# Performance work log

Measured on AMD Instinct MI355X. Metric: run time of the kernel, lower is better.

## Reference

```python
import jax, jax.numpy as jnp
import numpy as np

FP8_MAX = 448.0   # torch.finfo(float8_e4m3fn).max
BLK = 128         # block_size = [128, 128] for weights; [1, 128] for activations
E, H, I, T, TOPK = 8, 2048, 1408, 512, 2
FP8 = jnp.float8_e4m3fn


def fp8_round(x):
    """Round-trip through float8_e4m3fn (simulates .to(float8_e4m3fn))."""
    return jnp.clip(x, -FP8_MAX, FP8_MAX).astype(FP8).astype(jnp.float32)


def setup_inputs() -> dict:
    key = jax.random.key(0)
    ks = jax.random.split(key, 7)
    hidden_states = jax.random.normal(ks[0], (T, H), jnp.float32)
    top_k_index = jax.random.randint(ks[1], (T, TOPK), 0, E)
    top_k_weights = jax.random.uniform(ks[2], (T, TOPK), jnp.float32)
    # FP8 weight codes (stored as fp32 values exactly representable in e4m3fn)
    gate_up_proj = fp8_round(jax.random.normal(ks[3], (E, 2 * I, H), jnp.float32))
    gate_up_proj_scale_inv = jax.random.uniform(ks[4], (E, (2 * I) // BLK, H // BLK), jnp.float32, 1e-4, 1e-2)
    down_proj = fp8_round(jax.random.normal(ks[5], (E, H, I), jnp.float32))
    down_proj_scale_inv = jax.random.uniform(ks[6], (E, H // BLK, I // BLK), jnp.float32, 1e-4, 1e-2)
    return {
        "hidden_states": hidden_states,
        "top_k_index": top_k_index,
        "top_k_weights": top_k_weights,
        "gate_up_proj": gate_up_proj,
        "gate_up_proj_scale_inv": gate_up_proj_scale_inv,
        "down_proj": down_proj,
        "down_proj_scale_inv": down_proj_scale_inv,
    }


def dequant_weight(wq, s):
    # wq: [E, N, K] fp8 codes; s: [E, N//BLK, K//BLK] per-128x128-block scale_inv
    e, n, k = wq.shape
    wb = wq.reshape(e, n // BLK, BLK, k // BLK, BLK)
    return (wb * s[:, :, None, :, None]).reshape(e, n, k)


def quant_dequant_act(x):
    # dynamic per-(row, 128-block) fp8 activation quantization, then dequant
    shp = x.shape
    xb = x.reshape(shp[:-1] + (shp[-1] // BLK, BLK))
    amax = jnp.max(jnp.abs(xb), axis=-1, keepdims=True)
    scale = jnp.maximum(amax, 1e-12) / FP8_MAX
    q = fp8_round(xb / scale)
    return (q * scale).reshape(shp)


def reference(hidden_states, top_k_index, top_k_weights, gate_up_proj,
              gate_up_proj_scale_inv, down_proj, down_proj_scale_inv):
    w_gu = dequant_weight(gate_up_proj, gate_up_proj_scale_inv)  # [E, 2I, H]
    w_d = dequant_weight(down_proj, down_proj_scale_inv)         # [E, H, I]
    # activation quantization is per-token-block, so unrouted tokens are
    # unaffected; dense per-expert compute + combine-weight mask equals the
    # original gather/scatter loop exactly (unrouted contributions weight 0).
    x = quant_dequant_act(hidden_states)                         # [T, H]
    gate_up = jnp.einsum('th,enh->etn', x, w_gu)                 # [E, T, 2I]
    gate, up = jnp.split(gate_up, 2, axis=-1)
    h = jax.nn.silu(gate) * up                                   # [E, T, I]
    h = quant_dequant_act(h)
    down = jnp.einsum('eti,ehi->eth', h, w_d)                    # [E, T, H]
    # combine[t, e] = sum over top-k slots routing token t to expert e
    combine = jnp.sum(jax.nn.one_hot(top_k_index, E, dtype=top_k_weights.dtype)
                      * top_k_weights[..., None], axis=1)        # [T, E]
    out = jnp.einsum('eth,te->th', down, combine)
    return out.astype(hidden_states.dtype)
```

## Files before the change

### kernel.cpp

```cpp
#include <hip/hip_runtime.h>
#include <math.h>

#define NE 8
#define HD 2048
#define ID 1408
#define NT 512
#define FP8MAX 448.0f

typedef __attribute__((ext_vector_type(4))) float floatx4;

__device__ __forceinline__ floatx4 fzero4() {
    floatx4 z; z.x = 0.f; z.y = 0.f; z.z = 0.f; z.w = 0.f; return z;
}

#define OFF_OFFS  0
#define OFF_TOK   1024
#define OFF_WGT   8192
#define OFF_ENT   16384
#define OFF_XSG   32768
#define OFF_XG    131072
#define OFF_HS    (3*1024*1024)
#define OFF_HQ    (3*1024*1024 + 65536)
#define OFF_GU0   (5*1024*1024)
#define OFF_GU1   (17*1024*1024)

#define LDA 136

__global__ void route_kernel(const int* __restrict__ tki,
                             const float* __restrict__ tkw,
                             int* __restrict__ offs,
                             int* __restrict__ tok,
                             float* __restrict__ wgt,
                             int* __restrict__ ent) {
    __shared__ int cnt[NE];
    __shared__ int cur[NE];
    __shared__ int base[NE + 1];
    int tid = threadIdx.x;
    if (tid < NE) { cnt[tid] = 0; cur[tid] = 0; }
    __syncthreads();
    int e = tki[tid];
    atomicAdd(&cnt[e], 1);
    __syncthreads();
    if (tid == 0) {
        int s = 0;
        for (int i = 0; i < NE; i++) { base[i] = s; s += cnt[i]; }
        base[NE] = s;
    }
    __syncthreads();
    int pos = atomicAdd(&cur[e], 1);
    int j = base[e] + pos;
    tok[j] = tid >> 1;
    wgt[j] = tkw[tid];
    ent[tid] = j;
    if (tid <= NE) offs[tid] = base[tid];
}

__global__ void quant_x_kernel(const float* __restrict__ x,
                               const int* __restrict__ ent,
                               unsigned char* __restrict__ xg,
                               float* __restrict__ xsg) {
    int wid = (blockIdx.x * 256 + threadIdx.x) >> 6;
    int lane = threadIdx.x & 63;
    int t = wid >> 4;
    int b = wid & 15;
    const float2 v = *(const float2*)(x + (long)t * HD + b * 128 + lane * 2);
    float am = fmaxf(fabsf(v.x), fabsf(v.y));
    #pragma unroll
    for (int m = 32; m; m >>= 1) am = fmaxf(am, __shfl_xor(am, m));
    float scale = fmaxf(am, 1e-12f) / FP8MAX;
    int p = __builtin_amdgcn_cvt_pk_fp8_f32(v.x / scale, v.y / scale, 0, false);
    unsigned short pk = (unsigned short)(p & 0xffff);
    int e0 = ent[2 * t], e1 = ent[2 * t + 1];
    *(unsigned short*)(xg + (long)e0 * HD + b * 128 + lane * 2) = pk;
    *(unsigned short*)(xg + (long)e1 * HD + b * 128 + lane * 2) = pk;
    if (lane == 0) { xsg[e0 * 16 + b] = scale; xsg[e1 * 16 + b] = scale; }
}

__global__ void quant_h_kernel(const float* __restrict__ gu0,
                               const float* __restrict__ gu1,
                               unsigned char* __restrict__ hq,
                               float* __restrict__ hs) {
    int wid = (blockIdx.x * 256 + threadIdx.x) >> 6;
    int lane = threadIdx.x & 63;
    int j = wid / 11;
    int b = wid - j * 11;
    long base = (long)j * 2816 + b * 128 + lane * 2;
    float2 ga = *(const float2*)(gu0 + base);
    float2 gb = *(const float2*)(gu1 + base);
    float2 ua = *(const float2*)(gu0 + base + 1408);
    float2 ub = *(const float2*)(gu1 + base + 1408);
    float gx = ga.x + gb.x, gy = ga.y + gb.y;
    float ux = ua.x + ub.x, uy = ua.y + ub.y;
    float hx = (gx / (1.0f + expf(-gx))) * ux;
    float hy = (gy / (1.0f + expf(-gy))) * uy;
    float am = fmaxf(fabsf(hx), fabsf(hy));
    #pragma unroll
    for (int m = 32; m; m >>= 1) am = fmaxf(am, __shfl_xor(am, m));
    float scale = fmaxf(am, 1e-12f) / FP8MAX;
    int p = __builtin_amdgcn_cvt_pk_fp8_f32(hx / scale, hy / scale, 0, false);
    *(unsigned short*)(hq + (long)j * ID + b * 128 + lane * 2) =
        (unsigned short)(p & 0xffff);
    if (lane == 0) hs[j * 11 + b] = scale;
}

__global__ __launch_bounds__(256, 4) void gemm1_kernel(
    const unsigned char* __restrict__ xg,
    const float* __restrict__ xsg,
    const float* __restrict__ wgu,
    const float* __restrict__ sgu,
    const int* __restrict__ offs,
    float* __restrict__ gu0,
    float* __restrict__ gu1) {
    int e = blockIdx.z;
    int jb = blockIdx.x >> 1;
    int kh = blockIdx.x & 1;
    int o0 = offs[e], o1 = offs[e + 1];
    int ne = o1 - o0;
    if (ne <= 0) return;

    __shared__ __align__(16) unsigned char Asm[128 * LDA];
    __shared__ __align__(16) unsigned char Bsm[64 * LDA];
    __shared__ __align__(16) float sxa[128 * 20];

    int tid = threadIdx.x;
    int wave = tid >> 6;
    int lane = tid & 63;
    int lr = lane & 15;
    int lq = lane >> 4;

    int bcol = tid & 31;
    int brow0 = tid >> 5;
    const float* bG = wgu + ((long)e * 2816 + jb * 32 + brow0) * HD + bcol * 4;
    const float* bU = wgu + ((long)e * 2816 + 1408 + jb * 32 + brow0) * HD + bcol * 4;
    const float* sgp = sgu + (e * 22 + (jb >> 2)) * 16;
    const float* sup = sgu + (e * 22 + 11 + (jb >> 2)) * 16;

    int aseg = tid & 7;
    int arow0 = tid >> 3;
    int kbS = kh * 8, kbE = kbS + 8;

    for (int m0 = 0; m0 < ne; m0 += 128) {
        int rem = ne - m0;
        int j0 = o0 + m0;

        {
            int r = tid >> 1, q = tid & 1;
            int j = j0 + r; if (j >= o1) j = o0;
            float4 s0 = *(const float4*)(xsg + j * 16 + q * 8);
            float4 s1 = *(const float4*)(xsg + j * 16 + q * 8 + 4);
            *(float4*)&sxa[r * 20 + q * 8] = s0;
            *(float4*)&sxa[r * 20 + q * 8 + 4] = s1;
        }

        const unsigned char* aBase0;
        const unsigned char* aBase1;
        const unsigned char* aBase2;
        const unsigned char* aBase3;
        {
            int j;
            j = j0 + arow0;       if (j >= o1) j = o0; aBase0 = xg + (long)j * HD + aseg * 16;
            j = j0 + 32 + arow0;  if (j >= o1) j = o0; aBase1 = xg + (long)j * HD + aseg * 16;
            j = j0 + 64 + arow0;  if (j >= o1) j = o0; aBase2 = xg + (long)j * HD + aseg * 16;
            j = j0 + 96 + arow0;  if (j >= o1) j = o0; aBase3 = xg + (long)j * HD + aseg * 16;
        }

        floatx4 facc[8];
        #pragma unroll
        for (int i = 0; i < 8; i++) facc[i] = fzero4();

        for (int kb = kbS; kb < kbE; kb++) {
            {
                uint4 a0 = *(const uint4*)(aBase0 + kb * 128);
                uint4 a1 = *(const uint4*)(aBase1 + kb * 128);
                uint4 a2 = *(const uint4*)(aBase2 + kb * 128);
                uint4 a3 = *(const uint4*)(aBase3 + kb * 128);
                float4 f0 = *(const float4*)(bG + kb * 128);
                float4 f1 = *(const float4*)(bG + kb * 128 + 8 * HD);
                float4 f2 = *(const float4*)(bG + kb * 128 + 16 * HD);
                float4 f3 = *(const float4*)(bG + kb * 128 + 24 * HD);
                float4 f4 = *(const float4*)(bU + kb * 128);
                float4 f5 = *(const float4*)(bU + kb * 128 + 8 * HD);
                float4 f6 = *(const float4*)(bU + kb * 128 + 16 * HD);
                float4 f7 = *(const float4*)(bU + kb * 128 + 24 * HD);
                *(uint4*)(&Asm[(arow0)      * LDA + aseg * 16]) = a0;
                *(uint4*)(&Asm[(arow0 + 32) * LDA + aseg * 16]) = a1;
                *(uint4*)(&Asm[(arow0 + 64) * LDA + aseg * 16]) = a2;
                *(uint4*)(&Asm[(arow0 + 96) * LDA + aseg * 16]) = a3;
                int p0 = __builtin_amdgcn_cvt_pk_fp8_f32(f0.x, f0.y, 0, false);
                p0 = __builtin_amdgcn_cvt_pk_fp8_f32(f0.z, f0.w, p0, true);
                int p1 = __builtin_amdgcn_cvt_pk_fp8_f32(f1.x, f1.y, 0, false);
                p1 = __builtin_amdgcn_cvt_pk_fp8_f32(f1.z, f1.w, p1, true);
                int p2 = __builtin_amdgcn_cvt_pk_fp8_f32(f2.x, f2.y, 0, false);
                p2 = __builtin_amdgcn_cvt_pk_fp8_f32(f2.z, f2.w, p2, true);
                int p3 = __builtin_amdgcn_cvt_pk_fp8_f32(f3.x, f3.y, 0, false);
                p3 = __builtin_amdgcn_cvt_pk_fp8_f32(f3.z, f3.w, p3, true);
                int p4 = __builtin_amdgcn_cvt_pk_fp8_f32(f4.x, f4.y, 0, false);
                p4 = __builtin_amdgcn_cvt_pk_fp8_f32(f4.z, f4.w, p4, true);
                int p5 = __builtin_amdgcn_cvt_pk_fp8_f32(f5.x, f5.y, 0, false);
                p5 = __builtin_amdgcn_cvt_pk_fp8_f32(f5.z, f5.w, p5, true);
                int p6 = __builtin_amdgcn_cvt_pk_fp8_f32(f6.x, f6.y, 0, false);
                p6 = __builtin_amdgcn_cvt_pk_fp8_f32(f6.z, f6.w, p6, true);
                int p7 = __builtin_amdgcn_cvt_pk_fp8_f32(f7.x, f7.y, 0, false);
                p7 = __builtin_amdgcn_cvt_pk_fp8_f32(f7.z, f7.w, p7, true);
                *(unsigned int*)(&Bsm[(brow0)      * LDA + bcol * 4]) = (unsigned int)p0;
                *(unsigned int*)(&Bsm[(brow0 + 8)  * LDA + bcol * 4]) = (unsigned int)p1;
                *(unsigned int*)(&Bsm[(brow0 + 16) * LDA + bcol * 4]) = (unsigned int)p2;
                *(unsigned int*)(&Bsm[(brow0 + 24) * LDA + bcol * 4]) = (unsigned int)p3;
                *(unsigned int*)(&Bsm[(brow0 + 32) * LDA + bcol * 4]) = (unsigned int)p4;
                *(unsigned int*)(&Bsm[(brow0 + 40) * LDA + bcol * 4]) = (unsigned int)p5;
                *(unsigned int*)(&Bsm[(brow0 + 48) * LDA + bcol * 4]) = (unsigned int)p6;
                *(unsigned int*)(&Bsm[(brow0 + 56) * LDA + bcol * 4]) = (unsigned int)p7;
            }
            __syncthreads();
            floatx4 cacc[8];
            #pragma unroll
            for (int i = 0; i < 8; i++) cacc[i] = fzero4();
            #pragma unroll
            for (int ks = 0; ks < 4; ks++) {
                long a[2], b[4];
                #pragma unroll
                for (int mi = 0; mi < 2; mi++)
                    a[mi] = *(const long*)(&Asm[(wave * 32 + mi * 16 + lr) * LDA + ks * 32 + lq * 8]);
                #pragma unroll
                for (int ni = 0; ni < 4; ni++)
                    b[ni] = *(const long*)(&Bsm[(ni * 16 + lr) * LDA + ks * 32 + lq * 8]);
                #pragma unroll
                for (int mi = 0; mi < 2; mi++)
                    #pragma unroll
                    for (int ni = 0; ni < 4; ni++)
                        cacc[mi * 4 + ni] = __builtin_amdgcn_mfma_f32_16x16x32_fp8_fp8(
                            a[mi], b[ni], cacc[mi * 4 + ni], 0, 0, 0);
            }
            float sg = sgp[kb];
            float su = sup[kb];
            #pragma unroll
            for (int mi = 0; mi < 2; mi++) {
                #pragma unroll
                for (int reg = 0; reg < 4; reg++) {
                    float sx = sxa[(wave * 32 + mi * 16 + lq * 4 + reg) * 20 + kb];
                    #pragma unroll
                    for (int ni = 0; ni < 4; ni++) {
                        float sw = (ni < 2) ? sg : su;
                        facc[mi * 4 + ni][reg] += cacc[mi * 4 + ni][reg] * (sw * sx);
                    }
                }
            }
            __syncthreads();
        }

        float* gu = kh ? gu1 : gu0;
        #pragma unroll
        for (int mi = 0; mi < 2; mi++) {
            #pragma unroll
            for (int ni = 0; ni < 4; ni++) {
                #pragma unroll
                for (int reg = 0; reg < 4; reg++) {
                    int r = wave * 32 + mi * 16 + lq * 4 + reg;
                    if (r < rem) {
                        long base = (long)(j0 + r) * 2816;
                        long col = (ni < 2) ? (jb * 32 + ni * 16 + lr)
                                            : (1408 + jb * 32 + (ni - 2) * 16 + lr);
                        gu[base + col] = facc[mi * 4 + ni][reg];
                    }
                }
            }
        }
    }
}

__global__ __launch_bounds__(256, 4) void gemm2_kernel(
    const unsigned char* __restrict__ hq,
    const float* __restrict__ hs,
    const float* __restrict__ wd,
    const float* __restrict__ sd,
    const int* __restrict__ offs,
    float* __restrict__ d0,
    float* __restrict__ d1) {
    int e = blockIdx.z;
    int jb = blockIdx.x >> 1;
    int kh = blockIdx.x & 1;
    int o0 = offs[e], o1 = offs[e + 1];
    int ne = o1 - o0;
    if (ne <= 0) return;

    __shared__ __align__(16) unsigned char Asm[128 * LDA];
    __shared__ __align__(16) unsigned char Bsm[32 * LDA];
    __shared__ __align__(16) float sha[128 * 12];

    int tid = threadIdx.x;
    int wave = tid >> 6;
    int lane = tid & 63;
    int lr = lane & 15;
    int lq = lane >> 4;

    int aseg = tid & 7;
    int arow0 = tid >> 3;

    int bcol = tid & 31;
    int brow0 = tid >> 5;
    const float* bB = wd + ((long)e * HD + jb * 32 + brow0) * ID + bcol * 4;
    const float* sdp = sd + (e * 16 + (jb >> 2)) * 11;

    int kb0 = kh ? 6 : 0, kb1 = kh ? 11 : 6;
    float* dp = kh ? d1 : d0;

    for (int m0 = 0; m0 < ne; m0 += 128) {
        int rem = ne - m0;
        int j0 = o0 + m0;

        if (tid < 128) {
            int j = j0 + tid;
            if (j >= o1) j = o0;
            const float* s = hs + j * 11;
            #pragma unroll
            for (int k = 0; k < 11; k++) sha[tid * 12 + k] = s[k];
        }

        const unsigned char* aBase0;
        const unsigned char* aBase1;
        const unsigned char* aBase2;
        const unsigned char* aBase3;
        {
            int j;
            j = j0 + arow0;       if (j >= o1) j = o0; aBase0 = hq + (long)j * ID + aseg * 16;
            j = j0 + 32 + arow0;  if (j >= o1) j = o0; aBase1 = hq + (long)j * ID + aseg * 16;
            j = j0 + 64 + arow0;  if (j >= o1) j = o0; aBase2 = hq + (long)j * ID + aseg * 16;
            j = j0 + 96 + arow0;  if (j >= o1) j = o0; aBase3 = hq + (long)j * ID + aseg * 16;
        }

        floatx4 facc[4];
        #pragma unroll
        for (int i = 0; i < 4; i++) facc[i] = fzero4();

        for (int kb = kb0; kb < kb1; kb++) {
            {
                uint4 a0 = *(const uint4*)(aBase0 + kb * 128);
                uint4 a1 = *(const uint4*)(aBase1 + kb * 128);
                uint4 a2 = *(const uint4*)(aBase2 + kb * 128);
                uint4 a3 = *(const uint4*)(aBase3 + kb * 128);
                float4 f0 = *(const float4*)(bB + kb * 128);
                float4 f1 = *(const float4*)(bB + kb * 128 + 8 * ID);
                float4 f2 = *(const float4*)(bB + kb * 128 + 16 * ID);
                float4 f3 = *(const float4*)(bB + kb * 128 + 24 * ID);
                *(uint4*)(&Asm[(arow0)      * LDA + aseg * 16]) = a0;
                *(uint4*)(&Asm[(arow0 + 32) * LDA + aseg * 16]) = a1;
                *(uint4*)(&Asm[(arow0 + 64) * LDA + aseg * 16]) = a2;
                *(uint4*)(&Asm[(arow0 + 96) * LDA + aseg * 16]) = a3;
                int p0 = __builtin_amdgcn_cvt_pk_fp8_f32(f0.x, f0.y, 0, false);
                p0 = __builtin_amdgcn_cvt_pk_fp8_f32(f0.z, f0.w, p0, true);
                int p1 = __builtin_amdgcn_cvt_pk_fp8_f32(f1.x, f1.y, 0, false);
                p1 = __builtin_amdgcn_cvt_pk_fp8_f32(f1.z, f1.w, p1, true);
                int p2 = __builtin_amdgcn_cvt_pk_fp8_f32(f2.x, f2.y, 0, false);
                p2 = __builtin_amdgcn_cvt_pk_fp8_f32(f2.z, f2.w, p2, true);
                int p3 = __builtin_amdgcn_cvt_pk_fp8_f32(f3.x, f3.y, 0, false);
                p3 = __builtin_amdgcn_cvt_pk_fp8_f32(f3.z, f3.w, p3, true);
                *(unsigned int*)(&Bsm[(brow0)      * LDA + bcol * 4]) = (unsigned int)p0;
                *(unsigned int*)(&Bsm[(brow0 + 8)  * LDA + bcol * 4]) = (unsigned int)p1;
                *(unsigned int*)(&Bsm[(brow0 + 16) * LDA + bcol * 4]) = (unsigned int)p2;
                *(unsigned int*)(&Bsm[(brow0 + 24) * LDA + bcol * 4]) = (unsigned int)p3;
            }
            __syncthreads();
            floatx4 cacc[4];
            #pragma unroll
            for (int i = 0; i < 4; i++) cacc[i] = fzero4();
            #pragma unroll
            for (int ks = 0; ks < 4; ks++) {
                long a[2], b[2];
                #pragma unroll
                for (int mi = 0; mi < 2; mi++)
                    a[mi] = *(const long*)(&Asm[(wave * 32 + mi * 16 + lr) * LDA + ks * 32 + lq * 8]);
                #pragma unroll
                for (int ni = 0; ni < 2; ni++)
                    b[ni] = *(const long*)(&Bsm[(ni * 16 + lr) * LDA + ks * 32 + lq * 8]);
                #pragma unroll
                for (int mi = 0; mi < 2; mi++)
                    #pragma unroll
                    for (int ni = 0; ni < 2; ni++)
                        cacc[mi * 2 + ni] = __builtin_amdgcn_mfma_f32_16x16x32_fp8_fp8(
                            a[mi], b[ni], cacc[mi * 2 + ni], 0, 0, 0);
            }
            float sw = sdp[kb];
            #pragma unroll
            for (int mi = 0; mi < 2; mi++) {
                #pragma unroll
                for (int reg = 0; reg < 4; reg++) {
                    float sh = sha[(wave * 32 + mi * 16 + lq * 4 + reg) * 12 + kb];
                    #pragma unroll
                    for (int ni = 0; ni < 2; ni++)
                        facc[mi * 2 + ni][reg] += cacc[mi * 2 + ni][reg] * (sw * sh);
                }
            }
            __syncthreads();
        }

        #pragma unroll
        for (int mi = 0; mi < 2; mi++) {
            #pragma unroll
            for (int ni = 0; ni < 2; ni++) {
                #pragma unroll
                for (int reg = 0; reg < 4; reg++) {
                    int r = wave * 32 + mi * 16 + lq * 4 + reg;
                    if (r < rem) {
                        dp[(long)(j0 + r) * HD + jb * 32 + ni * 16 + lr] =
                            facc[mi * 2 + ni][reg];
                    }
                }
            }
        }
    }
}

__global__ void combine_kernel(const float* __restrict__ d0,
                               const float* __restrict__ d1,
                               const int* __restrict__ ent,
                               const float* __restrict__ tkw,
                               float* __restrict__ out) {
    int gid = blockIdx.x * 256 + threadIdx.x;
    int t = gid >> 9;
    int c4 = gid & 511;
    int j0 = ent[2 * t], j1 = ent[2 * t + 1];
    float w0 = tkw[2 * t], w1 = tkw[2 * t + 1];
    long b0 = (long)j0 * HD + c4 * 4;
    long b1 = (long)j1 * HD + c4 * 4;
    float4 a0 = *(const float4*)(d0 + b0);
    float4 a1 = *(const float4*)(d1 + b0);
    float4 a2 = *(const float4*)(d0 + b1);
    float4 a3 = *(const float4*)(d1 + b1);
    float4 r;
    r.x = w0 * (a0.x + a1.x) + w1 * (a2.x + a3.x);
    r.y = w0 * (a0.y + a1.y) + w1 * (a2.y + a3.y);
    r.z = w0 * (a0.z + a1.z) + w1 * (a2.z + a3.z);
    r.w = w0 * (a0.w + a1.w) + w1 * (a2.w + a3.w);
    *(float4*)(out + (long)t * HD + c4 * 4) = r;
}

extern "C" void kernel_launch(void* const* d_in, const int* in_sizes, int n_in,
                              void* d_out, int out_size, void* d_ws, size_t ws_size,
                              hipStream_t stream) {
    (void)in_sizes; (void)n_in; (void)out_size; (void)ws_size;
    const float* x   = (const float*)d_in[0];
    const int*   tki = (const int*)d_in[1];
    const float* tkw = (const float*)d_in[2];
    const float* wgu = (const float*)d_in[3];
    const float* sgu = (const float*)d_in[4];
    const float* wd  = (const float*)d_in[5];
    const float* sd  = (const float*)d_in[6];
    float* out = (float*)d_out;
    char* ws = (char*)d_ws;

    int*   offs = (int*)(ws + OFF_OFFS);
    int*   tok  = (int*)(ws + OFF_TOK);
    float* wgt  = (float*)(ws + OFF_WGT);
    int*   ent  = (int*)(ws + OFF_ENT);
    float* xsg  = (float*)(ws + OFF_XSG);
    unsigned char* xg = (unsigned char*)(ws + OFF_XG);
    float* hs   = (float*)(ws + OFF_HS);
    unsigned char* hq = (unsigned char*)(ws + OFF_HQ);
    float* gu0  = (float*)(ws + OFF_GU0);
    float* gu1  = (float*)(ws + OFF_GU1);
    float* dp0  = (float*)(ws + OFF_GU0);
    float* dp1  = (float*)(ws + OFF_GU1);

    route_kernel<<<1, 1024, 0, stream>>>(tki, tkw, offs, tok, wgt, ent);
    quant_x_kernel<<<2048, 256, 0, stream>>>(x, ent, xg, xsg);
    gemm1_kernel<<<dim3(88, 1, NE), 256, 0, stream>>>(xg, xsg, wgu, sgu, offs, gu0, gu1);
    quant_h_kernel<<<2816, 256, 0, stream>>>(gu0, gu1, hq, hs);
    gemm2_kernel<<<dim3(128, 1, NE), 256, 0, stream>>>(hq, hs, wd, sd, offs, dp0, dp1);
    combine_kernel<<<1024, 256, 0, stream>>>(dp0, dp1, ent, tkw, out);
}
```

Before: 381.3 us.

## Pre-convert weights to fp8 in a separate pass and split M tiles across the grid

Adds a grid-stride kernel that converts both fp32 weight tensors to packed fp8 in workspace on every call. Both GEMMs then load 16-byte fp8 rows directly instead of fp32 loads plus in-loop conversion. The serial per-expert M-tile loop is replaced by a grid y dimension of 8 tiles, which adds more blocks for parallelism. The trade-off is one extra full pass over the weights, reading about 276 MB of fp32 and writing fp8, plus extra workspace.

```diff
diff --git a/kernel.cpp b/kernel.cpp
--- a/kernel.cpp
+++ b/kernel.cpp
@@ -23,6 +23,8 @@
 #define OFF_HQ    (3*1024*1024 + 65536)
 #define OFF_GU0   (5*1024*1024)
 #define OFF_GU1   (17*1024*1024)
+#define OFF_WGU8  (29L*1024*1024)
+#define OFF_WD8   (76L*1024*1024)
 
 #define LDA 136
 
@@ -55,6 +57,29 @@
     if (tid <= NE) offs[tid] = base[tid];
 }
 
+__global__ void quant_w_kernel(const float* __restrict__ wgu,
+                               const float* __restrict__ wd,
+                               unsigned int* __restrict__ wgu8,
+                               unsigned int* __restrict__ wd8) {
+    const long NGU4 = (long)NE * 2816 * 2048 / 4;
+    const long ND4  = (long)NE * HD * ID / 4;
+    long stride = (long)gridDim.x * 256;
+    for (long i = (long)blockIdx.x * 256 + threadIdx.x; i < NGU4 + ND4; i += stride) {
+        if (i < NGU4) {
+            float4 v = ((const float4*)wgu)[i];
+            int p = __builtin_amdgcn_cvt_pk_fp8_f32(v.x, v.y, 0, false);
+            p = __builtin_amdgcn_cvt_pk_fp8_f32(v.z, v.w, p, true);
+            wgu8[i] = (unsigned int)p;
+        } else {
+            long k = i - NGU4;
+            float4 v = ((const float4*)wd)[k];
+            int p = __builtin_amdgcn_cvt_pk_fp8_f32(v.x, v.y, 0, false);
+            p = __builtin_amdgcn_cvt_pk_fp8_f32(v.z, v.w, p, true);
+            wd8[k] = (unsigned int)p;
+        }
+    }
+}
+
 __global__ void quant_x_kernel(const float* __restrict__ x,
                                const int* __restrict__ ent,
                                unsigned char* __restrict__ xg,
@@ -106,162 +131,131 @@
 __global__ __launch_bounds__(256, 4) void gemm1_kernel(
     const unsigned char* __restrict__ xg,
     const float* __restrict__ xsg,
-    const float* __restrict__ wgu,
+    const unsigned char* __restrict__ wgu8,
     const float* __restrict__ sgu,
     const int* __restrict__ offs,
     float* __restrict__ gu0,
     float* __restrict__ gu1) {
     int e = blockIdx.z;
+    int mt = blockIdx.y;
     int jb = blockIdx.x >> 1;
     int kh = blockIdx.x & 1;
     int o0 = offs[e], o1 = offs[e + 1];
     int ne = o1 - o0;
-    if (ne <= 0) return;
+    int m0 = mt * 128;
+    if (m0 >= ne) return;
+    int rem = ne - m0;
+    int j0 = o0 + m0;
 
     __shared__ __align__(16) unsigned char Asm[128 * LDA];
     __shared__ __align__(16) unsigned char Bsm[64 * LDA];
     __shared__ __align__(16) float sxa[128 * 20];
 
     int tid = threadIdx.x;
+    {
+        int r = tid >> 1, q = tid & 1;
+        int j = j0 + r; if (j >= o1) j = o0;
+        float4 s0 = *(const float4*)(xsg + j * 16 + q * 8);
+        float4 s1 = *(const float4*)(xsg + j * 16 + q * 8 + 4);
+        *(float4*)&sxa[r * 20 + q * 8] = s0;
+        *(float4*)&sxa[r * 20 + q * 8 + 4] = s1;
+    }
+
     int wave = tid >> 6;
     int lane = tid & 63;
     int lr = lane & 15;
     int lq = lane >> 4;
 
-    int bcol = tid & 31;
-    int brow0 = tid >> 5;
-    const float* bG = wgu + ((long)e * 2816 + jb * 32 + brow0) * HD + bcol * 4;
-    const float* bU = wgu + ((long)e * 2816 + 1408 + jb * 32 + brow0) * HD + bcol * 4;
+    int aseg = tid & 7;
+    int arow0 = tid >> 3;
+    const unsigned char* aBase0;
+    const unsigned char* aBase1;
+    const unsigned char* aBase2;
+    const unsigned char* aBase3;
+    {
+        int j;
+        j = j0 + arow0;       if (j >= o1) j = o0; aBase0 = xg + (long)j * HD + aseg * 16;
+        j = j0 + 32 + arow0;  if (j >= o1) j = o0; aBase1 = xg + (long)j * HD + aseg * 16;
+        j = j0 + 64 + arow0;  if (j >= o1) j = o0; aBase2 = xg + (long)j * HD + aseg * 16;
+        j = j0 + 96 + arow0;  if (j >= o1) j = o0; aBase3 = xg + (long)j * HD + aseg * 16;
+    }
+
+    const unsigned char* bG8 = wgu8 + ((long)e * 2816 + jb * 32 + arow0) * HD + aseg * 16;
+    const unsigned char* bU8 = wgu8 + ((long)e * 2816 + 1408 + jb * 32 + arow0) * HD + aseg * 16;
     const float* sgp = sgu + (e * 22 + (jb >> 2)) * 16;
     const float* sup = sgu + (e * 22 + 11 + (jb >> 2)) * 16;
 
-    int aseg = tid & 7;
-    int arow0 = tid >> 3;
+    floatx4 facc[8];
+    #pragma unroll
+    for (int i = 0; i < 8; i++) facc[i] = fzero4();
+
     int kbS = kh * 8, kbE = kbS + 8;
 
-    for (int m0 = 0; m0 < ne; m0 += 128) {
-        int rem = ne - m0;
-        int j0 = o0 + m0;
-
+    for (int kb = kbS; kb < kbE; kb++) {
         {
-            int r = tid >> 1, q = tid & 1;
-            int j = j0 + r; if (j >= o1) j = o0;
-            float4 s0 = *(const float4*)(xsg + j * 16 + q * 8);
-            float4 s1 = *(const float4*)(xsg + j * 16 + q * 8 + 4);
-            *(float4*)&sxa[r * 20 + q * 8] = s0;
-            *(float4*)&sxa[r * 20 + q * 8 + 4] = s1;
-        }
-
-        const unsigned char* aBase0;
-        const unsigned char* aBase1;
-        const unsigned char* aBase2;
-        const unsigned char* aBase3;
-        {
-            int j;
-            j = j0 + arow0;       if (j >= o1) j = o0; aBase0 = xg + (long)j * HD + aseg * 16;
-            j = j0 + 32 + arow0;  if (j >= o1) j = o0; aBase1 = xg + (long)j * HD + aseg * 16;
-            j = j0 + 64 + arow0;  if (j >= o1) j = o0; aBase2 = xg + (long)j * HD + aseg * 16;
-            j = j0 + 96 + arow0;  if (j >= o1) j = o0; aBase3 = xg + (long)j * HD + aseg * 16;
-        }
-
-        floatx4 facc[8];
-        #pragma unroll
-        for (int i = 0; i < 8; i++) facc[i] = fzero4();
-
-        for (int kb = kbS; kb < kbE; kb++) {
-            {
-                uint4 a0 = *(const uint4*)(aBase0 + kb * 128);
-                uint4 a1 = *(const uint4*)(aBase1 + kb * 128);
-                uint4 a2 = *(const uint4*)(aBase2 + kb * 128);
-                uint4 a3 = *(const uint4*)(aBase3 + kb * 128);
-                float4 f0 = *(const float4*)(bG + kb * 128);
-                float4 f1 = *(const float4*)(bG + kb * 128 + 8 * HD);
-                float4 f2 = *(const float4*)(bG + kb * 128 + 16 * HD);
-                float4 f3 = *(const float4*)(bG + kb * 128 + 24 * HD);
-                float4 f4 = *(const float4*)(bU + kb * 128);
-                float4 f5 = *(const float4*)(bU + kb * 128 + 8 * HD);
-                float4 f6 = *(const float4*)(bU + kb * 128 + 16 * HD);
-                float4 f7 = *(const float4*)(bU + kb * 128 + 24 * HD);
-                *(uint4*)(&Asm[(arow0)      * LDA + aseg * 16]) = a0;
-                *(uint4*)(&Asm[(arow0 + 32) * LDA + aseg * 16]) = a1;
-                *(uint4*)(&Asm[(arow0 + 64) * LDA + aseg * 16]) = a2;
-                *(uint4*)(&Asm[(arow0 + 96) * LDA + aseg * 16]) = a3;
-                int p0 = __builtin_amdgcn_cvt_pk_fp8_f32(f0.x, f0.y, 0, false);
-                p0 = __builtin_amdgcn_cvt_pk_fp8_f32(f0.z, f0.w, p0, true);
-                int p1 = __builtin_amdgcn_cvt_pk_fp8_f32(f1.x, f1.y, 0, false);
-                p1 = __builtin_amdgcn_cvt_pk_fp8_f32(f1.z, f1.w, p1, true);
-                int p2 = __builtin_amdgcn_cvt_pk_fp8_f32(f2.x, f2.y, 0, false);
-                p2 = __builtin_amdgcn_cvt_pk_fp8_f32(f2.z, f2.w, p2, true);
-                int p3 = __builtin_amdgcn_cvt_pk_fp8_f32(f3.x, f3.y, 0, false);
-                p3 = __builtin_amdgcn_cvt_pk_fp8_f32(f3.z, f3.w, p3, true);
-                int p4 = __builtin_amdgcn_cvt_pk_fp8_f32(f4.x, f4.y, 0, false);
-                p4 = __builtin_amdgcn_cvt_pk_fp8_f32(f4.z, f4.w, p4, true);
-                int p5 = __builtin_amdgcn_cvt_pk_fp8_f32(f5.x, f5.y, 0, false);
-                p5 = __builtin_amdgcn_cvt_pk_fp8_f32(f5.z, f5.w, p5, true);
-                int p6 = __builtin_amdgcn_cvt_pk_fp8_f32(f6.x, f6.y, 0, false);
-                p6 = __builtin_amdgcn_cvt_pk_fp8_f32(f6.z, f6.w, p6, true);
-                int p7 = __builtin_amdgcn_cvt_pk_fp8_f32(f7.x, f7.y, 0, false);
-                p7 = __builtin_amdgcn_cvt_pk_fp8_f32(f7.z, f7.w, p7, true);
-                *(unsigned int*)(&Bsm[(brow0)      * LDA + bcol * 4]) = (unsigned int)p0;
-                *(unsigned int*)(&Bsm[(brow0 + 8)  * LDA + bcol * 4]) = (unsigned int)p1;
-                *(unsigned int*)(&Bsm[(brow0 + 16) * LDA + bcol * 4]) = (unsigned int)p2;
-                *(unsigned int*)(&Bsm[(brow0 + 24) * LDA + bcol * 4]) = (unsigned int)p3;
-                *(unsigned int*)(&Bsm[(brow0 + 32) * LDA + bcol * 4]) = (unsigned int)p4;
-                *(unsigned int*)(&Bsm[(brow0 + 40) * LDA + bcol * 4]) = (unsigned int)p5;
-                *(unsigned int*)(&Bsm[(brow0 + 48) * LDA + bcol * 4]) = (unsigned int)p6;
-                *(unsigned int*)(&Bsm[(brow0 + 56) * LDA + bcol * 4]) = (unsigned int)p7;
-            }
-            __syncthreads();
-            floatx4 cacc[8];
-            #pragma unroll
-            for (int i = 0; i < 8; i++) cacc[i] = fzero4();
-            #pragma unroll
-            for (int ks = 0; ks < 4; ks++) {
-                long a[2], b[4];
-                #pragma unroll
-                for (int mi = 0; mi < 2; mi++)
-                    a[mi] = *(const long*)(&Asm[(wave * 32 + mi * 16 + lr) * LDA + ks * 32 + lq * 8]);
+            uint4 a0 = *(const uint4*)(aBase0 + kb * 128);
+            uint4 a1 = *(const uint4*)(aBase1 + kb * 128);
+            uint4 a2 = *(const uint4*)(aBase2 + kb * 128);
+            uint4 a3 = *(const uint4*)(aBase3 + kb * 128);
+            uint4 b0 = *(const uint4*)(bG8 + kb * 128);
+            uint4 b1 = *(const uint4*)(bU8 + kb * 128);
+            *(uint4*)(&Asm[(arow0)      * LDA + aseg * 16]) = a0;
+            *(uint4*)(&Asm[(arow0 + 32) * LDA + aseg * 16]) = a1;
+            *(uint4*)(&Asm[(arow0 + 64) * LDA + aseg * 16]) = a2;
+            *(uint4*)(&Asm[(arow0 + 96) * LDA + aseg * 16]) = a3;
+            *(uint4*)(&Bsm[(arow0)      * LDA + aseg * 16]) = b0;
+            *(uint4*)(&Bsm[(arow0 + 32) * LDA + aseg * 16]) = b1;
+        }
+        __syncthreads();
+        floatx4 cacc[8];
+        #pragma unroll
+        for (int i = 0; i < 8; i++) cacc[i] = fzero4();
+        #pragma unroll
+        for (int ks = 0; ks < 4; ks++) {
+            long a[2], b[4];
+            #pragma unroll
+            for (int mi = 0; mi < 2; mi++)
+                a[mi] = *(const long*)(&Asm[(wave * 32 + mi * 16 + lr) * LDA + ks * 32 + lq * 8]);
+            #pragma unroll
+            for (int ni = 0; ni < 4; ni++)
+                b[ni] = *(const long*)(&Bsm[(ni * 16 + lr) * LDA + ks * 32 + lq * 8]);
+            #pragma unroll
+            for (int mi = 0; mi < 2; mi++)
                 #pragma unroll
                 for (int ni = 0; ni < 4; ni++)
-                    b[ni] = *(const long*)(&Bsm[(ni * 16 + lr) * LDA + ks * 32 + lq * 8]);
+                    cacc[mi * 4 + ni] = __builtin_amdgcn_mfma_f32_16x16x32_fp8_fp8(
+                        a[mi], b[ni], cacc[mi * 4 + ni], 0, 0, 0);
+        }
+        float sg = sgp[kb];
+        float su = sup[kb];
+        #pragma unroll
+        for (int mi = 0; mi < 2; mi++) {
+            #pragma unroll
+            for (int reg = 0; reg < 4; reg++) {
+                float sx = sxa[(wave * 32 + mi * 16 + lq * 4 + reg) * 20 + kb];
                 #pragma unroll
-                for (int mi = 0; mi < 2; mi++)
-                    #pragma unroll
-                    for (int ni = 0; ni < 4; ni++)
-                        cacc[mi * 4 + ni] = __builtin_amdgcn_mfma_f32_16x16x32_fp8_fp8(
-                            a[mi], b[ni], cacc[mi * 4 + ni], 0, 0, 0);
-            }
-            float sg = sgp[kb];
-            float su = sup[kb];
-            #pragma unroll
-            for (int mi = 0; mi < 2; mi++) {
-                #pragma unroll
-                for (int reg = 0; reg < 4; reg++) {
-                    float sx = sxa[(wave * 32 + mi * 16 + lq * 4 + reg) * 20 + kb];
-                    #pragma unroll
-                    for (int ni = 0; ni < 4; ni++) {
-                        float sw = (ni < 2) ? sg : su;
-                        facc[mi * 4 + ni][reg] += cacc[mi * 4 + ni][reg] * (sw * sx);
-                    }
+                for (int ni = 0; ni < 4; ni++) {
+                    float sw = (ni < 2) ? sg : su;
+                    facc[mi * 4 + ni][reg] += cacc[mi * 4 + ni][reg] * (sw * sx);
                 }
             }
-            __syncthreads();
-        }
-
-        float* gu = kh ? gu1 : gu0;
-        #pragma unroll
-        for (int mi = 0; mi < 2; mi++) {
-            #pragma unroll
-            for (int ni = 0; ni < 4; ni++) {
-                #pragma unroll
-                for (int reg = 0; reg < 4; reg++) {
-                    int r = wave * 32 + mi * 16 + lq * 4 + reg;
-                    if (r < rem) {
-                        long base = (long)(j0 + r) * 2816;
-                        long col = (ni < 2) ? (jb * 32 + ni * 16 + lr)
-                                            : (1408 + jb * 32 + (ni - 2) * 16 + lr);
-                        gu[base + col] = facc[mi * 4 + ni][reg];
-                    }
+        }
+        __syncthreads();
+    }
+
+    float* gu = kh ? gu1 : gu0;
+    #pragma unroll
+    for (int mi = 0; mi < 2; mi++) {
+        #pragma unroll
+        for (int ni = 0; ni < 4; ni++) {
+            #pragma unroll
+            for (int reg = 0; reg < 4; reg++) {
+                int r = wave * 32 + mi * 16 + lq * 4 + reg;
+                if (r < rem) {
+                    long base = (long)(j0 + r) * 2816;
+                    long col = (ni < 2) ? (jb * 32 + ni * 16 + lr)
+                                        : (1408 + jb * 32 + (ni - 2) * 16 + lr);
+                    gu[base + col] = facc[mi * 4 + ni][reg];
                 }
             }
         }
@@ -271,23 +265,35 @@
 __global__ __launch_bounds__(256, 4) void gemm2_kernel(
     const unsigned char* __restrict__ hq,
     const float* __restrict__ hs,
-    const float* __restrict__ wd,
+    const unsigned char* __restrict__ wd8,
     const float* __restrict__ sd,
     const int* __restrict__ offs,
     float* __restrict__ d0,
     float* __restrict__ d1) {
     int e = blockIdx.z;
+    int mt = blockIdx.y;
     int jb = blockIdx.x >> 1;
     int kh = blockIdx.x & 1;
     int o0 = offs[e], o1 = offs[e + 1];
     int ne = o1 - o0;
-    if (ne <= 0) return;
+    int m0 = mt * 128;
+    if (m0 >= ne) return;
+    int rem = ne - m0;
+    int j0 = o0 + m0;
 
     __shared__ __align__(16) unsigned char Asm[128 * LDA];
     __shared__ __align__(16) unsigned char Bsm[32 * LDA];
     __shared__ __align__(16) float sha[128 * 12];
 
     int tid = threadIdx.x;
+    if (tid < 128) {
+        int j = j0 + tid;
+        if (j >= o1) j = o0;
+        const float* s = hs + j * 11;
+        #pragma unroll
+        for (int k = 0; k < 11; k++) sha[tid * 12 + k] = s[k];
+    }
+
     int wave = tid >> 6;
     int lane = tid & 63;
     int lr = lane & 15;
@@ -295,115 +301,85 @@
 
     int aseg = tid & 7;
     int arow0 = tid >> 3;
-
-    int bcol = tid & 31;
-    int brow0 = tid >> 5;
-    const float* bB = wd + ((long)e * HD + jb * 32 + brow0) * ID + bcol * 4;
+    const unsigned char* aBase0;
+    const unsigned char* aBase1;
+    const unsigned char* aBase2;
+    const unsigned char* aBase3;
+    {
+        int j;
+        j = j0 + arow0;       if (j >= o1) j = o0; aBase0 = hq + (long)j * ID + aseg * 16;
+        j = j0 + 32 + arow0;  if (j >= o1) j = o0; aBase1 = hq + (long)j * ID + aseg * 16;
+        j = j0 + 64 + arow0;  if (j >= o1) j = o0; aBase2 = hq + (long)j * ID + aseg * 16;
+        j = j0 + 96 + arow0;  if (j >= o1) j = o0; aBase3 = hq + (long)j * ID + aseg * 16;
+    }
+
+    const unsigned char* bB8 = wd8 + ((long)e * HD + jb * 32 + arow0) * ID + aseg * 16;
     const float* sdp = sd + (e * 16 + (jb >> 2)) * 11;
 
+    floatx4 facc[4];
+    #pragma unroll
+    for (int i = 0; i < 4; i++) facc[i] = fzero4();
+
     int kb0 = kh ? 6 : 0, kb1 = kh ? 11 : 6;
-    float* dp = kh ? d1 : d0;
-
-    for (int m0 = 0; m0 < ne; m0 += 128) {
-        int rem = ne - m0;
-        int j0 = o0 + m0;
-
-        if (tid < 128) {
-            int j = j0 + tid;
-            if (j >= o1) j = o0;
-            const float* s = hs + j * 11;
-            #pragma unroll
-            for (int k = 0; k < 11; k++) sha[tid * 12 + k] = s[k];
-        }
-
-        const unsigned char* aBase0;
-        const unsigned char* aBase1;
-        const unsigned char* aBase2;
-        const unsigned char* aBase3;
+
+    for (int kb = kb0; kb < kb1; kb++) {
         {
-            int j;
-            j = j0 + arow0;       if (j >= o1) j = o0; aBase0 = hq + (long)j * ID + aseg * 16;
-            j = j0 + 32 + arow0;  if (j >= o1) j = o0; aBase1 = hq + (long)j * ID + aseg * 16;
-            j = j0 + 64 + arow0;  if (j >= o1) j = o0; aBase2 = hq + (long)j * ID + aseg * 16;
-            j = j0 + 96 + arow0;  if (j >= o1) j = o0; aBase3 = hq + (long)j * ID + aseg * 16;
-        }
-
-        floatx4 facc[4];
-        #pragma unroll
-        for (int i = 0; i < 4; i++) facc[i] = fzero4();
-
-        for (int kb = kb0; kb < kb1; kb++) {
-            {
-                uint4 a0 = *(const uint4*)(aBase0 + kb * 128);
-                uint4 a1 = *(const uint4*)(aBase1 + kb * 128);
-                uint4 a2 = *(const uint4*)(aBase2 + kb * 128);
-                uint4 a3 = *(const uint4*)(aBase3 + kb * 128);
-                float4 f0 = *(const float4*)(bB + kb * 128);
-                float4 f1 = *(const float4*)(bB + kb * 128 + 8 * ID);
-                float4 f2 = *(const float4*)(bB + kb * 128 + 16 * ID);
-                float4 f3 = *(const float4*)(bB + kb * 128 + 24 * ID);
-                *(uint4*)(&Asm[(arow0)      * LDA + aseg * 16]) = a0;
-                *(uint4*)(&Asm[(arow0 + 32) * LDA + aseg * 16]) = a1;
-                *(uint4*)(&Asm[(arow0 + 64) * LDA + aseg * 16]) = a2;
-                *(uint4*)(&Asm[(arow0 + 96) * LDA + aseg * 16]) = a3;
-                int p0 = __builtin_amdgcn_cvt_pk_fp8_f32(f0.x, f0.y, 0, false);
-                p0 = __builtin_amdgcn_cvt_pk_fp8_f32(f0.z, f0.w, p0, true);
-                int p1 = __builtin_amdgcn_cvt_pk_fp8_f32(f1.x, f1.y, 0, false);
-                p1 = __builtin_amdgcn_cvt_pk_fp8_f32(f1.z, f1.w, p1, true);
-                int p2 = __builtin_amdgcn_cvt_pk_fp8_f32(f2.x, f2.y, 0, false);
-                p2 = __builtin_amdgcn_cvt_pk_fp8_f32(f2.z, f2.w, p2, true);
-                int p3 = __builtin_amdgcn_cvt_pk_fp8_f32(f3.x, f3.y, 0, false);
-                p3 = __builtin_amdgcn_cvt_pk_fp8_f32(f3.z, f3.w, p3, true);
-                *(unsigned int*)(&Bsm[(brow0)      * LDA + bcol * 4]) = (unsigned int)p0;
-                *(unsigned int*)(&Bsm[(brow0 + 8)  * LDA + bcol * 4]) = (unsigned int)p1;
-                *(unsigned int*)(&Bsm[(brow0 + 16) * LDA + bcol * 4]) = (unsigned int)p2;
-                *(unsigned int*)(&Bsm[(brow0 + 24) * LDA + bcol * 4]) = (unsigned int)p3;
-            }
-            __syncthreads();
-            floatx4 cacc[4];
-            #pragma unroll
-            for (int i = 0; i < 4; i++) cacc[i] = fzero4();
-            #pragma unroll
-            for (int ks = 0; ks < 4; ks++) {
-                long a[2], b[2];
-                #pragma unroll
-                for (int mi = 0; mi < 2; mi++)
-                    a[mi] = *(const long*)(&Asm[(wave * 32 + mi * 16 + lr) * LDA + ks * 32 + lq * 8]);
+            uint4 a0 = *(const uint4*)(aBase0 + kb * 128);
+            uint4 a1 = *(const uint4*)(aBase1 + kb * 128);
+            uint4 a2 = *(const uint4*)(aBase2 + kb * 128);
+            uint4 a3 = *(const uint4*)(aBase3 + kb * 128);
+            uint4 b0 = *(const uint4*)(bB8 + kb * 128);
+            *(uint4*)(&Asm[(arow0)      * LDA + aseg * 16]) = a0;
+            *(uint4*)(&Asm[(arow0 + 32) * LDA + aseg * 16]) = a1;
+            *(uint4*)(&Asm[(arow0 + 64) * LDA + aseg * 16]) = a2;
+            *(uint4*)(&Asm[(arow0 + 96) * LDA + aseg * 16]) = a3;
+            *(uint4*)(&Bsm[(arow0)      * LDA + aseg * 16]) = b0;
+        }
+        __syncthreads();
+        floatx4 cacc[4];
+        #pragma unroll
+        for (int i = 0; i < 4; i++) cacc[i] = fzero4();
+        #pragma unroll
+        for (int ks = 0; ks < 4; ks++) {
+            long a[2], b[2];
+            #pragma unroll
+            for (int mi = 0; mi < 2; mi++)
+                a[mi] = *(const long*)(&Asm[(wave * 32 + mi * 16 + lr) * LDA + ks * 32 + lq * 8]);
+            #pragma unroll
+            for (int ni = 0; ni < 2; ni++)
+                b[ni] = *(const long*)(&Bsm[(ni * 16 + lr) * LDA + ks * 32 + lq * 8]);
+            #pragma unroll
+            for (int mi = 0; mi < 2; mi++)
                 #pragma unroll
                 for (int ni = 0; ni < 2; ni++)
-                    b[ni] = *(const long*)(&Bsm[(ni * 16 + lr) * LDA + ks * 32 + lq * 8]);
+                    cacc[mi * 2 + ni] = __builtin_amdgcn_mfma_f32_16x16x32_fp8_fp8(
+                        a[mi], b[ni], cacc[mi * 2 + ni], 0, 0, 0);
+        }
+        float sw = sdp[kb];
+        #pragma unroll
+        for (int mi = 0; mi < 2; mi++) {
+            #pragma unroll
+            for (int reg = 0; reg < 4; reg++) {
+                float sh = sha[(wave * 32 + mi * 16 + lq * 4 + reg) * 12 + kb];
                 #pragma unroll
-                for (int mi = 0; mi < 2; mi++)
-                    #pragma unroll
-                    for (int ni = 0; ni < 2; ni++)
-                        cacc[mi * 2 + ni] = __builtin_amdgcn_mfma_f32_16x16x32_fp8_fp8(
-                            a[mi], b[ni], cacc[mi * 2 + ni], 0, 0, 0);
+                for (int ni = 0; ni < 2; ni++)
+                    facc[mi * 2 + ni][reg] += cacc[mi * 2 + ni][reg] * (sw * sh);
             }
-            float sw = sdp[kb];
-            #pragma unroll
-            for (int mi = 0; mi < 2; mi++) {
-                #pragma unroll
-                for (int reg = 0; reg < 4; reg++) {
-                    float sh = sha[(wave * 32 + mi * 16 + lq * 4 + reg) * 12 + kb];
-                    #pragma unroll
-                    for (int ni = 0; ni < 2; ni++)
-                        facc[mi * 2 + ni][reg] += cacc[mi * 2 + ni][reg] * (sw * sh);
-                }
-            }
-            __syncthreads();
-        }
-
-        #pragma unroll
-        for (int mi = 0; mi < 2; mi++) {
-            #pragma unroll
-            for (int ni = 0; ni < 2; ni++) {
-                #pragma unroll
-                for (int reg = 0; reg < 4; reg++) {
-                    int r = wave * 32 + mi * 16 + lq * 4 + reg;
-                    if (r < rem) {
-                        dp[(long)(j0 + r) * HD + jb * 32 + ni * 16 + lr] =
-                            facc[mi * 2 + ni][reg];
-                    }
+        }
+        __syncthreads();
+    }
+
+    float* dp = kh ? d1 : d0;
+    #pragma unroll
+    for (int mi = 0; mi < 2; mi++) {
+        #pragma unroll
+        for (int ni = 0; ni < 2; ni++) {
+            #pragma unroll
+            for (int reg = 0; reg < 4; reg++) {
+                int r = wave * 32 + mi * 16 + lq * 4 + reg;
+                if (r < rem) {
+                    dp[(long)(j0 + r) * HD + jb * 32 + ni * 16 + lr] =
+                        facc[mi * 2 + ni][reg];
                 }
             }
         }
@@ -458,13 +434,17 @@
     unsigned char* hq = (unsigned char*)(ws + OFF_HQ);
     float* gu0  = (float*)(ws + OFF_GU0);
     float* gu1  = (float*)(ws + OFF_GU1);
+    unsigned char* wgu8 = (unsigned char*)(ws + OFF_WGU8);
+    unsigned char* wd8  = (unsigned char*)(ws + OFF_WD8);
     float* dp0  = (float*)(ws + OFF_GU0);
     float* dp1  = (float*)(ws + OFF_GU1);
 
     route_kernel<<<1, 1024, 0, stream>>>(tki, tkw, offs, tok, wgt, ent);
+    quant_w_kernel<<<2048, 256, 0, stream>>>(wgu, wd, (unsigned int*)wgu8,
+                                             (unsigned int*)wd8);
     quant_x_kernel<<<2048, 256, 0, stream>>>(x, ent, xg, xsg);
-    gemm1_kernel<<<dim3(88, 1, NE), 256, 0, stream>>>(xg, xsg, wgu, sgu, offs, gu0, gu1);
+    gemm1_kernel<<<dim3(88, 8, NE), 256, 0, stream>>>(xg, xsg, wgu8, sgu, offs, gu0, gu1);
     quant_h_kernel<<<2816, 256, 0, stream>>>(gu0, gu1, hq, hs);
-    gemm2_kernel<<<dim3(128, 1, NE), 256, 0, stream>>>(hq, hs, wd, sd, offs, dp0, dp1);
+    gemm2_kernel<<<dim3(128, 8, NE), 256, 0, stream>>>(hq, hs, wd8, sd, offs, dp0, dp1);
     combine_kernel<<<1024, 256, 0, stream>>>(dp0, dp1, ent, tkw, out);
 }
```

After: 541.3 us. 41.9% more time.
